# Optimization experiments

Hardware: AMD Instinct MI355X
Metric: run time of the kernel (lower is better)

## Reference

```python
import jax, jax.numpy as jnp
import numpy as np

USER_COUNT = 100000
ITEM_COUNT = 50000
LATENT = 64
N_LAYERS = 3
NEG_SLOPE = 0.2


def _xavier(key, shape):
    fan_in, fan_out = shape[-2], shape[-1]
    lim = jnp.sqrt(6.0 / (fan_in + fan_out))
    return jax.random.uniform(key, shape, jnp.float32, -lim, lim)


def setup_inputs() -> dict:
    key = jax.random.key(0)
    ks = jax.random.split(key, 20)
    E = 2400000
    edge_index = jax.random.randint(ks[0], (2, E), 0, USER_COUNT + ITEM_COUNT, dtype=jnp.int64)
    user = jax.random.randint(ks[1], (4096,), 0, USER_COUNT, dtype=jnp.int64)
    item = jax.random.randint(ks[2], (4096,), 0, ITEM_COUNT, dtype=jnp.int64)
    inp = {"user": user, "item": item, "edge_index": edge_index}
    # online encoder params
    inp["user_emb_o"] = _xavier(ks[3], (USER_COUNT, LATENT))
    inp["item_emb_o"] = _xavier(ks[4], (ITEM_COUNT, LATENT))
    inp["W_o"] = _xavier(ks[5], (N_LAYERS, LATENT, LATENT))
    inp["att_src_o"] = _xavier(ks[6], (N_LAYERS, 1, LATENT))[:, 0, :]
    inp["att_dst_o"] = _xavier(ks[7], (N_LAYERS, 1, LATENT))[:, 0, :]
    inp["bias_o"] = jnp.zeros((N_LAYERS, LATENT), jnp.float32)
    # target encoder params (momentum copy; frozen in torch)
    inp["user_emb_t"] = _xavier(ks[8], (USER_COUNT, LATENT))
    inp["item_emb_t"] = _xavier(ks[9], (ITEM_COUNT, LATENT))
    inp["W_t"] = _xavier(ks[10], (N_LAYERS, LATENT, LATENT))
    inp["att_src_t"] = _xavier(ks[11], (N_LAYERS, 1, LATENT))[:, 0, :]
    inp["att_dst_t"] = _xavier(ks[12], (N_LAYERS, 1, LATENT))[:, 0, :]
    inp["bias_t"] = jnp.zeros((N_LAYERS, LATENT), jnp.float32)
    # predictor Linear(latent, latent)
    inp["pred_W"] = _xavier(ks[13], (LATENT, LATENT))
    inp["pred_b"] = jnp.zeros((LATENT,), jnp.float32)
    return inp


def _gat_conv(x, src, dst, n_nodes, W, a_src, a_dst, b):
    # PyG GATConv, heads=1, concat=True, add_self_loops handled by caller.
    h = x @ W                                   # [N, F]
    e = jax.nn.leaky_relu(jnp.take(h @ a_src, src) + jnp.take(h @ a_dst, dst), NEG_SLOPE)  # [E]
    m = jax.ops.segment_max(e, dst, num_segments=n_nodes)
    m = jnp.where(jnp.isfinite(m), m, 0.0)
    ex = jnp.exp(e - jnp.take(m, dst))
    den = jax.ops.segment_sum(ex, dst, num_segments=n_nodes)
    alpha = ex / jnp.take(den, dst)             # softmax over incoming edges per dst
    msg = alpha[:, None] * jnp.take(h, src, axis=0)  # [E, F]
    return jax.ops.segment_sum(msg, dst, num_segments=n_nodes) + b


def _encode(user_emb, item_emb, W, a_src, a_dst, bias, src, dst):
    x = jnp.concatenate([user_emb, item_emb], axis=0)  # [N, F]
    n_nodes = x.shape[0]
    for l in range(N_LAYERS):
        x = _gat_conv(x, src, dst, n_nodes, W[l], a_src[l], a_dst[l], bias[l])
    return x[:user_emb.shape[0]], x[user_emb.shape[0]:]


def reference(user_emb_o, item_emb_o, W_o, att_src_o, att_dst_o, bias_o,
              user_emb_t, item_emb_t, W_t, att_src_t, att_dst_t, bias_t,
              pred_W, pred_b, user, item, edge_index):
    n_nodes = user_emb_o.shape[0] + item_emb_o.shape[0]
    loops = jnp.arange(n_nodes, dtype=edge_index.dtype)
    src = jnp.concatenate([edge_index[0], loops])  # add self loops (PyG default)
    dst = jnp.concatenate([edge_index[1], loops])
    u_all_o, i_all_o = _encode(user_emb_o, item_emb_o, W_o, att_src_o, att_dst_o, bias_o, src, dst)
    u_all_t, i_all_t = _encode(user_emb_t, item_emb_t, W_t, att_src_t, att_dst_t, bias_t, src, dst)
    u_online = jnp.take(u_all_o, user, axis=0)
    i_online = jnp.take(i_all_o, item, axis=0)
    u_target = jnp.take(u_all_t, user, axis=0)
    i_target = jnp.take(i_all_t, item, axis=0)
    return (u_online @ pred_W.T + pred_b, u_target, i_online @ pred_W.T + pred_b, i_target)
```

## Files before the change

kernel.cpp:

```cpp
#include <hip/hip_runtime.h>
#include <math.h>
#include <stdint.h>

#define LAT 64
#define SLICE 16384
#define BIN_CHUNK 1024

static inline int cdiv(int a, int b) { return (a + b - 1) / b; }

__global__ void k_scan1(const int* __restrict__ cnt, int N, int* __restrict__ out, int* __restrict__ blk_sums) {
    __shared__ int sdata[256];
    int t = threadIdx.x, b = blockIdx.x;
    int base = b * 1024 + t * 4;
    int v[4];
    int s = 0;
#pragma unroll
    for (int u = 0; u < 4; u++) { int i = base + u; v[u] = (i < N) ? cnt[i] : 0; s += v[u]; }
    sdata[t] = s; __syncthreads();
    for (int off = 1; off < 256; off <<= 1) {
        int x = (t >= off) ? sdata[t - off] : 0;
        __syncthreads();
        sdata[t] += x;
        __syncthreads();
    }
    int run = sdata[t] - s;
#pragma unroll
    for (int u = 0; u < 4; u++) { int i = base + u; if (i < N) out[i] = run; run += v[u]; }
    if (t == 255) blk_sums[b] = sdata[255];
}

__global__ void k_scan2(int* __restrict__ blk_sums, int NB) {
    __shared__ int sdata[256];
    int t = threadIdx.x;
    int v = (t < NB) ? blk_sums[t] : 0;
    sdata[t] = v; __syncthreads();
    for (int off = 1; off < 256; off <<= 1) {
        int x = (t >= off) ? sdata[t - off] : 0;
        __syncthreads();
        sdata[t] += x;
        __syncthreads();
    }
    if (t < NB) blk_sums[t] = sdata[t] - v;
}

__global__ void k_scan3(int* __restrict__ row_ptr, const int* __restrict__ blk_offs, int N, int ET) {
    int t = threadIdx.x, b = blockIdx.x;
    int base = b * 1024 + t * 4;
    int off = blk_offs[b];
#pragma unroll
    for (int u = 0; u < 4; u++) { int i = base + u; if (i < N) row_ptr[i] += off; }
    if (b == 0 && t == 0) row_ptr[N] = ET;
}

__global__ __launch_bounds__(256) void k_l0(
        const float* __restrict__ ueo, const float* __restrict__ ieo,
        const float* __restrict__ uet, const float* __restrict__ iet, int NU,
        const float* __restrict__ Wo, const float* __restrict__ Wt,
        const float* __restrict__ atso, const float* __restrict__ atdo,
        const float* __restrict__ atst, const float* __restrict__ atdt,
        float* __restrict__ h2, float* __restrict__ asp, float* __restrict__ adp, int N,
        int gemmGrid, int binGrid,
        const int* __restrict__ src_arr, const int* __restrict__ dst_arr,
        int E, int ET, int rsz, int bcap,
        int2* __restrict__ buckets, int* __restrict__ gcur, int* __restrict__ cnt) {
    __shared__ float sW[64 * 64];
    __shared__ float sX[128 * 65];
    __shared__ float sAs[64], sAd[64];
    int t = threadIdx.x;

    if ((int)blockIdx.x >= gemmGrid) {
        int* lcnt = (int*)sW;
        int* lbase = (int*)sW + 8;
        int bb = blockIdx.x - gemmGrid;
        for (int base = bb * BIN_CHUNK; base < ET; base += binGrid * BIN_CHUNK) {
            if (t < 8) lcnt[t] = 0;
            __syncthreads();
            int s[4], d[4], r[4], lofs[4];
            int nval = 0;
            if (base + BIN_CHUNK <= E) {
                int4 s4 = ((const int4*)(src_arr + base))[t];
                int4 d4 = ((const int4*)(dst_arr + base))[t];
                s[0] = s4.x; s[1] = s4.y; s[2] = s4.z; s[3] = s4.w;
                d[0] = d4.x; d[1] = d4.y; d[2] = d4.z; d[3] = d4.w;
                nval = 4;
            } else {
                for (int k = 0; k < 4; k++) {
                    int e = base + t * 4 + k;
                    if (e < ET) {
                        if (e < E) { s[nval] = src_arr[e]; d[nval] = dst_arr[e]; }
                        else { s[nval] = e - E; d[nval] = e - E; }
                        nval++;
                    }
                }
            }
            for (int k = 0; k < nval; k++) {
                r[k] = d[k] / rsz;
                lofs[k] = atomicAdd(&lcnt[r[k]], 1);
                atomicAdd(&cnt[d[k]], 1);
            }
            __syncthreads();
            if (t < 8) lbase[t] = atomicAdd(&gcur[t], lcnt[t]);
            __syncthreads();
            for (int k = 0; k < nval; k++) {
                buckets[(size_t)r[k] * bcap + lbase[r[k]] + lofs[k]] = make_int2(s[k], d[k]);
            }
            __syncthreads();
        }
        return;
    }

    int enc = blockIdx.x & 1;
    int bb = blockIdx.x >> 1;
    const float* ue = enc ? uet : ueo;
    const float* ie = enc ? iet : ieo;
    const float* W = enc ? Wt : Wo;
    const float* att_s = enc ? atst : atso;
    const float* att_d = enc ? atdt : atdo;
    float* h2e = h2 + enc * 64;
    int row0 = bb * 128;
    {
        const float4* Wv = (const float4*)W;
        float4* sWv = (float4*)sW;
#pragma unroll
        for (int u = 0; u < 4; u++) sWv[t + 256 * u] = Wv[t + 256 * u];
    }
    if (t < 64) { sAs[t] = att_s[t]; sAd[t] = att_d[t]; }
    {
#pragma unroll
        for (int u = 0; u < 8; u++) {
            int idx = t + 256 * u;
            int r = idx >> 4, c4 = idx & 15;
            int grow = row0 + r;
            float4 v = make_float4(0.f, 0.f, 0.f, 0.f);
            if (grow < N) {
                const float* base = (grow < NU) ? ue + (size_t)grow * 64 : ie + (size_t)(grow - NU) * 64;
                v = ((const float4*)base)[c4];
            }
            int cc = c4 * 4;
            sX[r * 65 + cc] = v.x; sX[r * 65 + cc + 1] = v.y; sX[r * 65 + cc + 2] = v.z; sX[r * 65 + cc + 3] = v.w;
        }
    }
    __syncthreads();
    int rl = t >> 2;
    int g = t & 3;
    int c0 = g * 16;
    int rA = rl * 2, rB = rA + 1;
    float accA[16], accB[16];
#pragma unroll
    for (int j = 0; j < 16; j++) { accA[j] = 0.f; accB[j] = 0.f; }
    for (int k = 0; k < 64; k++) {
        float xa = sX[rA * 65 + k];
        float xb = sX[rB * 65 + k];
        const float4* wr = (const float4*)&sW[k * 64 + c0];
        float4 w0 = wr[0], w1 = wr[1], w2 = wr[2], w3 = wr[3];
        accA[0] += xa * w0.x; accA[1] += xa * w0.y; accA[2] += xa * w0.z; accA[3] += xa * w0.w;
        accA[4] += xa * w1.x; accA[5] += xa * w1.y; accA[6] += xa * w1.z; accA[7] += xa * w1.w;
        accA[8] += xa * w2.x; accA[9] += xa * w2.y; accA[10] += xa * w2.z; accA[11] += xa * w2.w;
        accA[12] += xa * w3.x; accA[13] += xa * w3.y; accA[14] += xa * w3.z; accA[15] += xa * w3.w;
        accB[0] += xb * w0.x; accB[1] += xb * w0.y; accB[2] += xb * w0.z; accB[3] += xb * w0.w;
        accB[4] += xb * w1.x; accB[5] += xb * w1.y; accB[6] += xb * w1.z; accB[7] += xb * w1.w;
        accB[8] += xb * w2.x; accB[9] += xb * w2.y; accB[10] += xb * w2.z; accB[11] += xb * w2.w;
        accB[12] += xb * w3.x; accB[13] += xb * w3.y; accB[14] += xb * w3.z; accB[15] += xb * w3.w;
    }
    float sA = 0.f, dA = 0.f, sB = 0.f, dB = 0.f;
#pragma unroll
    for (int j = 0; j < 16; j++) {
        sA += accA[j] * sAs[c0 + j]; dA += accA[j] * sAd[c0 + j];
        sB += accB[j] * sAs[c0 + j]; dB += accB[j] * sAd[c0 + j];
    }
    sA += __shfl_xor(sA, 1); sA += __shfl_xor(sA, 2);
    dA += __shfl_xor(dA, 1); dA += __shfl_xor(dA, 2);
    sB += __shfl_xor(sB, 1); sB += __shfl_xor(sB, 2);
    dB += __shfl_xor(dB, 1); dB += __shfl_xor(dB, 2);
    int rowA = row0 + rA, rowB = row0 + rB;
    if (rowA < N) {
        if (g == 0) { asp[(size_t)rowA * 2 + enc] = sA; adp[(size_t)rowA * 2 + enc] = dA; }
        float4* hv = (float4*)&h2e[(size_t)rowA * 128 + c0];
        hv[0] = make_float4(accA[0], accA[1], accA[2], accA[3]);
        hv[1] = make_float4(accA[4], accA[5], accA[6], accA[7]);
        hv[2] = make_float4(accA[8], accA[9], accA[10], accA[11]);
        hv[3] = make_float4(accA[12], accA[13], accA[14], accA[15]);
    }
    if (rowB < N) {
        if (g == 0) { asp[(size_t)rowB * 2 + enc] = sB; adp[(size_t)rowB * 2 + enc] = dB; }
        float4* hv = (float4*)&h2e[(size_t)rowB * 128 + c0];
        hv[0] = make_float4(accB[0], accB[1], accB[2], accB[3]);
        hv[1] = make_float4(accB[4], accB[5], accB[6], accB[7]);
        hv[2] = make_float4(accB[8], accB[9], accB[10], accB[11]);
        hv[3] = make_float4(accB[12], accB[13], accB[14], accB[15]);
    }
}

__global__ __launch_bounds__(256) void k_binB(const int2* __restrict__ buckets, int bcap,
                                              const int* __restrict__ gcur,
                                              const int* __restrict__ row_ptr, int* __restrict__ cnt,
                                              int* __restrict__ csr_src) {
    int r = blockIdx.x & 7;
    int nb = blockIdx.x >> 3;
    int stride = (gridDim.x >> 3) * 256;
    int total = gcur[r];
    const int* bp = (const int*)(buckets + (size_t)r * bcap);
    for (int i = nb * 256 + threadIdx.x; i < total; i += stride) {
        int s = __builtin_nontemporal_load(bp + 2 * i);
        int d = __builtin_nontemporal_load(bp + 2 * i + 1);
        int pos = atomicAdd(&cnt[d], 1);
        csr_src[row_ptr[d] + pos] = s;
    }
}

__global__ __launch_bounds__(256) void k_gemm2m(const float* __restrict__ xo, const float* __restrict__ xt,
        int NU,
        const float* __restrict__ Wo, const float* __restrict__ Wt,
        const float* __restrict__ atso, const float* __restrict__ atdo,
        const float* __restrict__ atst, const float* __restrict__ atdt,
        float* __restrict__ h2, float* __restrict__ asp, float* __restrict__ adp, int N) {
    __shared__ float sW[64 * 64];
    __shared__ float sX[128 * 65];
    __shared__ float sAs[64], sAd[64];
    int enc = blockIdx.x & 1;
    int bb = blockIdx.x >> 1;
    const float* x = enc ? xt : xo;
    const float* W = enc ? Wt : Wo;
    const float* att_s = enc ? atst : atso;
    const float* att_d = enc ? atdt : atdo;
    float* h2e = h2 + enc * 64;
    int t = threadIdx.x;
    int row0 = bb * 128;
    {
        const float4* Wv = (const float4*)W;
        float4* sWv = (float4*)sW;
#pragma unroll
        for (int u = 0; u < 4; u++) sWv[t + 256 * u] = Wv[t + 256 * u];
    }
    if (t < 64) { sAs[t] = att_s[t]; sAd[t] = att_d[t]; }
    {
#pragma unroll
        for (int u = 0; u < 8; u++) {
            int idx = t + 256 * u;
            int r = idx >> 4, c4 = idx & 15;
            int grow = row0 + r;
            float4 v = make_float4(0.f, 0.f, 0.f, 0.f);
            if (grow < N) v = ((const float4*)(x + (size_t)grow * 64))[c4];
            int cc = c4 * 4;
            sX[r * 65 + cc] = v.x; sX[r * 65 + cc + 1] = v.y; sX[r * 65 + cc + 2] = v.z; sX[r * 65 + cc + 3] = v.w;
        }
    }
    __syncthreads();
    int rl = t >> 2;
    int g = t & 3;
    int c0 = g * 16;
    int rA = rl * 2, rB = rA + 1;
    float accA[16], accB[16];
#pragma unroll
    for (int j = 0; j < 16; j++) { accA[j] = 0.f; accB[j] = 0.f; }
    for (int k = 0; k < 64; k++) {
        float xa = sX[rA * 65 + k];
        float xb = sX[rB * 65 + k];
        const float4* wr = (const float4*)&sW[k * 64 + c0];
        float4 w0 = wr[0], w1 = wr[1], w2 = wr[2], w3 = wr[3];
        accA[0] += xa * w0.x; accA[1] += xa * w0.y; accA[2] += xa * w0.z; accA[3] += xa * w0.w;
        accA[4] += xa * w1.x; accA[5] += xa * w1.y; accA[6] += xa * w1.z; accA[7] += xa * w1.w;
        accA[8] += xa * w2.x; accA[9] += xa * w2.y; accA[10] += xa * w2.z; accA[11] += xa * w2.w;
        accA[12] += xa * w3.x; accA[13] += xa * w3.y; accA[14] += xa * w3.z; accA[15] += xa * w3.w;
        accB[0] += xb * w0.x; accB[1] += xb * w0.y; accB[2] += xb * w0.z; accB[3] += xb * w0.w;
        accB[4] += xb * w1.x; accB[5] += xb * w1.y; accB[6] += xb * w1.z; accB[7] += xb * w1.w;
        accB[8] += xb * w2.x; accB[9] += xb * w2.y; accB[10] += xb * w2.z; accB[11] += xb * w2.w;
        accB[12] += xb * w3.x; accB[13] += xb * w3.y; accB[14] += xb * w3.z; accB[15] += xb * w3.w;
    }
    float sA = 0.f, dA = 0.f, sB = 0.f, dB = 0.f;
#pragma unroll
    for (int j = 0; j < 16; j++) {
        sA += accA[j] * sAs[c0 + j]; dA += accA[j] * sAd[c0 + j];
        sB += accB[j] * sAs[c0 + j]; dB += accB[j] * sAd[c0 + j];
    }
    sA += __shfl_xor(sA, 1); sA += __shfl_xor(sA, 2);
    dA += __shfl_xor(dA, 1); dA += __shfl_xor(dA, 2);
    sB += __shfl_xor(sB, 1); sB += __shfl_xor(sB, 2);
    dB += __shfl_xor(dB, 1); dB += __shfl_xor(dB, 2);
    int rowA = row0 + rA, rowB = row0 + rB;
    if (rowA < N) {
        if (g == 0) { asp[(size_t)rowA * 2 + enc] = sA; adp[(size_t)rowA * 2 + enc] = dA; }
        float4* hv = (float4*)&h2e[(size_t)rowA * 128 + c0];
        hv[0] = make_float4(accA[0], accA[1], accA[2], accA[3]);
        hv[1] = make_float4(accA[4], accA[5], accA[6], accA[7]);
        hv[2] = make_float4(accA[8], accA[9], accA[10], accA[11]);
        hv[3] = make_float4(accA[12], accA[13], accA[14], accA[15]);
    }
    if (rowB < N) {
        if (g == 0) { asp[(size_t)rowB * 2 + enc] = sB; adp[(size_t)rowB * 2 + enc] = dB; }
        float4* hv = (float4*)&h2e[(size_t)rowB * 128 + c0];
        hv[0] = make_float4(accB[0], accB[1], accB[2], accB[3]);
        hv[1] = make_float4(accB[4], accB[5], accB[6], accB[7]);
        hv[2] = make_float4(accB[8], accB[9], accB[10], accB[11]);
        hv[3] = make_float4(accB[12], accB[13], accB[14], accB[15]);
    }
}

__global__ __launch_bounds__(256) void k_agg2(const float* __restrict__ h2,
                                              const int* __restrict__ row_ptr, const int* __restrict__ csr_src,
                                              const float2* __restrict__ asv, const float2* __restrict__ adv,
                                              const float* __restrict__ bias_o, const float* __restrict__ bias_t,
                                              float* __restrict__ xo, float* __restrict__ xt, int N,
                                              const int* __restrict__ selu, const int* __restrict__ seli,
                                              int nSel, int nSelU, int NU,
                                              float* __restrict__ selxo, float* __restrict__ outT_u,
                                              float* __restrict__ outT_i) {
    int wid = threadIdx.x >> 6, lane = threadIdx.x & 63;
    int r = blockIdx.x * 4 + wid;
    int d;
    float *po, *pt;
    if (selu) {
        if (r >= nSel) return;
        if (r < nSelU) { d = selu[r]; pt = outT_u + (size_t)r * 64; }
        else { int rr = r - nSelU; d = seli[rr] + NU; pt = outT_i + (size_t)rr * 64; }
        po = selxo + (size_t)r * 64;
    } else {
        if (r >= N) return;
        d = r;
        po = xo + (size_t)d * 64;
        pt = xt + (size_t)d * 64;
    }
    int s0 = row_ptr[d], s1 = row_ptr[d + 1];
    float2 advv = adv[d];
    int j0 = s0 + lane;
    int sv0 = 0; float eo0 = -1e30f, et0 = -1e30f;
    if (j0 < s1) {
        sv0 = csr_src[j0];
        float2 a2 = asv[sv0];
        float eo = a2.x + advv.x; eo0 = (eo > 0.f) ? eo : 0.2f * eo;
        float et = a2.y + advv.y; et0 = (et > 0.f) ? et : 0.2f * et;
    }
    float mo = eo0, mt = et0;
    for (int j = j0 + 64; j < s1; j += 64) {
        float2 a2 = asv[csr_src[j]];
        float eo = a2.x + advv.x; eo = (eo > 0.f) ? eo : 0.2f * eo; mo = fmaxf(mo, eo);
        float et = a2.y + advv.y; et = (et > 0.f) ? et : 0.2f * et; mt = fmaxf(mt, et);
    }
#pragma unroll
    for (int o = 32; o; o >>= 1) { mo = fmaxf(mo, __shfl_xor(mo, o)); mt = fmaxf(mt, __shfl_xor(mt, o)); }
    float exo0 = (j0 < s1) ? expf(eo0 - mo) : 0.f;
    float ext0 = (j0 < s1) ? expf(et0 - mt) : 0.f;
    float so = exo0, st = ext0;
    for (int j = j0 + 64; j < s1; j += 64) {
        float2 a2 = asv[csr_src[j]];
        float eo = a2.x + advv.x; eo = (eo > 0.f) ? eo : 0.2f * eo; so += expf(eo - mo);
        float et = a2.y + advv.y; et = (et > 0.f) ? et : 0.2f * et; st += expf(et - mt);
    }
#pragma unroll
    for (int o = 32; o; o >>= 1) { so += __shfl_xor(so, o); st += __shfl_xor(st, o); }
    float invo = 1.f / so, invt = 1.f / st;
    exo0 *= invo; ext0 *= invt;
    int sub = lane >> 4, c4 = lane & 15;
    float4 ao = make_float4(0.f, 0.f, 0.f, 0.f);
    float4 at4 = make_float4(0.f, 0.f, 0.f, 0.f);
    for (int cb = s0; cb < s1; cb += 64) {
        int sv; float wo, wt;
        if (cb == s0) { sv = sv0; wo = exo0; wt = ext0; }
        else {
            int jj = cb + lane; sv = 0; wo = 0.f; wt = 0.f;
            if (jj < s1) {
                sv = csr_src[jj];
                float2 a2 = asv[sv];
                float eo = a2.x + advv.x; eo = (eo > 0.f) ? eo : 0.2f * eo; wo = expf(eo - mo) * invo;
                float et = a2.y + advv.y; et = (et > 0.f) ? et : 0.2f * et; wt = expf(et - mt) * invt;
            }
        }
        int c = s1 - cb; if (c > 64) c = 64;
        int q = 0;
        for (; q + 8 <= c; q += 8) {
            int ilA = q + sub, ilB = q + 4 + sub;
            int sA = __shfl(sv, ilA), sB = __shfl(sv, ilB);
            float oA = __shfl(wo, ilA), oB = __shfl(wo, ilB);
            float tA = __shfl(wt, ilA), tB = __shfl(wt, ilB);
            const float* ha = h2 + (size_t)sA * 128 + (c4 << 2);
            const float* hb = h2 + (size_t)sB * 128 + (c4 << 2);
            float4 hoA = *(const float4*)ha;
            float4 htA = *(const float4*)(ha + 64);
            float4 hoB = *(const float4*)hb;
            float4 htB = *(const float4*)(hb + 64);
            ao.x += oA * hoA.x; ao.y += oA * hoA.y; ao.z += oA * hoA.z; ao.w += oA * hoA.w;
            at4.x += tA * htA.x; at4.y += tA * htA.y; at4.z += tA * htA.z; at4.w += tA * htA.w;
            ao.x += oB * hoB.x; ao.y += oB * hoB.y; ao.z += oB * hoB.z; ao.w += oB * hoB.w;
            at4.x += tB * htB.x; at4.y += tB * htB.y; at4.z += tB * htB.z; at4.w += tB * htB.w;
        }
        for (; q < c; q += 4) {
            int il = q + sub;
            int s = __shfl(sv, il);
            float o_ = __shfl(wo, il);
            float t_ = __shfl(wt, il);
            const float* hb = h2 + (size_t)s * 128 + (c4 << 2);
            float4 ho = *(const float4*)hb;
            float4 ht = *(const float4*)(hb + 64);
            ao.x += o_ * ho.x; ao.y += o_ * ho.y; ao.z += o_ * ho.z; ao.w += o_ * ho.w;
            at4.x += t_ * ht.x; at4.y += t_ * ht.y; at4.z += t_ * ht.z; at4.w += t_ * ht.w;
        }
    }
#pragma unroll
    for (int o = 16; o <= 32; o <<= 1) {
        ao.x += __shfl_xor(ao.x, o); ao.y += __shfl_xor(ao.y, o);
        ao.z += __shfl_xor(ao.z, o); ao.w += __shfl_xor(ao.w, o);
        at4.x += __shfl_xor(at4.x, o); at4.y += __shfl_xor(at4.y, o);
        at4.z += __shfl_xor(at4.z, o); at4.w += __shfl_xor(at4.w, o);
    }
    if (lane < 16) {
        float4 bo = ((const float4*)bias_o)[c4];
        ao.x += bo.x; ao.y += bo.y; ao.z += bo.z; ao.w += bo.w;
        ((float4*)po)[c4] = ao;
        float4 bt = ((const float4*)bias_t)[c4];
        at4.x += bt.x; at4.y += bt.y; at4.z += bt.z; at4.w += bt.w;
        ((float4*)pt)[c4] = at4;
    }
}

__global__ __launch_bounds__(256) void k_pred2(const float* __restrict__ x, int nU, int nI,
                                               const float* __restrict__ W, const float* __restrict__ bvec,
                                               float* __restrict__ outU, float* __restrict__ outI) {
    __shared__ float sWt[64 * 65];
    int t = threadIdx.x;
#pragma unroll
    for (int u = 0; u < 16; u++) {
        int i = u * 256 + t;
        int c = i >> 6, k = i & 63;
        sWt[k * 65 + c] = W[i];
    }
    __syncthreads();
    int wid = t >> 6, lane = t & 63;
    int r = blockIdx.x * 4 + wid;
    if (r >= nU + nI) return;
    float xr = x[(size_t)r * 64 + lane];
    float acc = bvec[lane];
    for (int k = 0; k < 64; k++)
        acc += __shfl(xr, k) * sWt[k * 65 + lane];
    float* dst = (r < nU) ? (outU + (size_t)r * 64) : (outI + (size_t)(r - nU) * 64);
    dst[lane] = acc;
}

__global__ void k_count(const int* __restrict__ dst_arr, int E, int N, int* __restrict__ cnt) {
    int e = blockIdx.x * blockDim.x + threadIdx.x;
    int ET = E + N;
    if (e < ET) {
        int d = (e < E) ? dst_arr[e] : (e - E);
        atomicAdd(&cnt[d], 1);
    }
}

__global__ void k_scatter(const int* __restrict__ src_arr, const int* __restrict__ dst_arr, int E, int N,
                          const int* __restrict__ row_ptr, int* __restrict__ cnt, int* __restrict__ csr_src) {
    int ET = E + N;
    int slice = blockIdx.x >> 3;
    int range = blockIdx.x & 7;
    int rsz = (N + 7) >> 3;
    int lo = range * rsz;
    int hi = lo + rsz; if (hi > N) hi = N;
    int base = slice * SLICE;
    int end = base + SLICE; if (end > ET) end = ET;
    for (int e = base + threadIdx.x; e < end; e += 256) {
        int s, d;
        if (e < E) { s = src_arr[e]; d = dst_arr[e]; }
        else { s = e - E; d = e - E; }
        if (d >= lo && d < hi) {
            int pos = atomicAdd(&cnt[d], 1);
            csr_src[row_ptr[d] + pos] = s;
        }
    }
}

__global__ __launch_bounds__(256) void k_gemm(const float* __restrict__ x,
                                              const float* __restrict__ ue, const float* __restrict__ ie, int NU,
                                              const float* __restrict__ W,
                                              const float* __restrict__ att_s, const float* __restrict__ att_d,
                                              float* __restrict__ h, float* __restrict__ as_, float* __restrict__ ad_,
                                              int N) {
    __shared__ float sW[64 * 64];
    __shared__ float sX[128 * 65];
    __shared__ float sAs[64], sAd[64];
    int t = threadIdx.x;
    int row0 = blockIdx.x * 128;
    {
        const float4* Wv = (const float4*)W;
        float4* sWv = (float4*)sW;
#pragma unroll
        for (int u = 0; u < 4; u++) sWv[t + 256 * u] = Wv[t + 256 * u];
    }
    if (t < 64) { sAs[t] = att_s[t]; sAd[t] = att_d[t]; }
    {
#pragma unroll
        for (int u = 0; u < 8; u++) {
            int idx = t + 256 * u;
            int r = idx >> 4, c4 = idx & 15;
            int grow = row0 + r;
            float4 v = make_float4(0.f, 0.f, 0.f, 0.f);
            if (grow < N) {
                const float* base = x ? (x + (size_t)grow * 64)
                                      : (grow < NU ? ue + (size_t)grow * 64 : ie + (size_t)(grow - NU) * 64);
                v = ((const float4*)base)[c4];
            }
            int cc = c4 * 4;
            sX[r * 65 + cc] = v.x; sX[r * 65 + cc + 1] = v.y; sX[r * 65 + cc + 2] = v.z; sX[r * 65 + cc + 3] = v.w;
        }
    }
    __syncthreads();
    int rl = t >> 2;
    int g = t & 3;
    int c0 = g * 16;
    int rA = rl * 2, rB = rA + 1;
    float accA[16], accB[16];
#pragma unroll
    for (int j = 0; j < 16; j++) { accA[j] = 0.f; accB[j] = 0.f; }
    for (int k = 0; k < 64; k++) {
        float xa = sX[rA * 65 + k];
        float xb = sX[rB * 65 + k];
        const float4* wr = (const float4*)&sW[k * 64 + c0];
        float4 w0 = wr[0], w1 = wr[1], w2 = wr[2], w3 = wr[3];
        accA[0] += xa * w0.x; accA[1] += xa * w0.y; accA[2] += xa * w0.z; accA[3] += xa * w0.w;
        accA[4] += xa * w1.x; accA[5] += xa * w1.y; accA[6] += xa * w1.z; accA[7] += xa * w1.w;
        accA[8] += xa * w2.x; accA[9] += xa * w2.y; accA[10] += xa * w2.z; accA[11] += xa * w2.w;
        accA[12] += xa * w3.x; accA[13] += xa * w3.y; accA[14] += xa * w3.z; accA[15] += xa * w3.w;
        accB[0] += xb * w0.x; accB[1] += xb * w0.y; accB[2] += xb * w0.z; accB[3] += xb * w0.w;
        accB[4] += xb * w1.x; accB[5] += xb * w1.y; accB[6] += xb * w1.z; accB[7] += xb * w1.w;
        accB[8] += xb * w2.x; accB[9] += xb * w2.y; accB[10] += xb * w2.z; accB[11] += xb * w2.w;
        accB[12] += xb * w3.x; accB[13] += xb * w3.y; accB[14] += xb * w3.z; accB[15] += xb * w3.w;
    }
    float sA = 0.f, dA = 0.f, sB = 0.f, dB = 0.f;
#pragma unroll
    for (int j = 0; j < 16; j++) {
        sA += accA[j] * sAs[c0 + j]; dA += accA[j] * sAd[c0 + j];
        sB += accB[j] * sAs[c0 + j]; dB += accB[j] * sAd[c0 + j];
    }
    sA += __shfl_xor(sA, 1); sA += __shfl_xor(sA, 2);
    dA += __shfl_xor(dA, 1); dA += __shfl_xor(dA, 2);
    sB += __shfl_xor(sB, 1); sB += __shfl_xor(sB, 2);
    dB += __shfl_xor(dB, 1); dB += __shfl_xor(dB, 2);
    int rowA = row0 + rA, rowB = row0 + rB;
    if (rowA < N) {
        if (g == 0) { as_[rowA] = sA; ad_[rowA] = dA; }
        float4* hv = (float4*)&h[(size_t)rowA * 64 + c0];
        hv[0] = make_float4(accA[0], accA[1], accA[2], accA[3]);
        hv[1] = make_float4(accA[4], accA[5], accA[6], accA[7]);
        hv[2] = make_float4(accA[8], accA[9], accA[10], accA[11]);
        hv[3] = make_float4(accA[12], accA[13], accA[14], accA[15]);
    }
    if (rowB < N) {
        if (g == 0) { as_[rowB] = sB; ad_[rowB] = dB; }
        float4* hv = (float4*)&h[(size_t)rowB * 64 + c0];
        hv[0] = make_float4(accB[0], accB[1], accB[2], accB[3]);
        hv[1] = make_float4(accB[4], accB[5], accB[6], accB[7]);
        hv[2] = make_float4(accB[8], accB[9], accB[10], accB[11]);
        hv[3] = make_float4(accB[12], accB[13], accB[14], accB[15]);
    }
}

__global__ __launch_bounds__(256) void k_agg(const float* __restrict__ h,
                                             const int* __restrict__ row_ptr, const int* __restrict__ csr_src,
                                             const float* __restrict__ as_, const float* __restrict__ ad_,
                                             const float* __restrict__ bias, float* __restrict__ xout, int N) {
    int wid = threadIdx.x >> 6, lane = threadIdx.x & 63;
    int d = blockIdx.x * 4 + wid;
    if (d >= N) return;
    int s0 = row_ptr[d], s1 = row_ptr[d + 1];
    float adv = ad_[d];
    int j0 = s0 + lane;
    int sv0 = 0; float ev0 = -1e30f;
    if (j0 < s1) {
        sv0 = csr_src[j0];
        float e = as_[sv0] + adv;
        ev0 = (e > 0.f) ? e : 0.2f * e;
    }
    float m = ev0;
    for (int j = j0 + 64; j < s1; j += 64) {
        float e = as_[csr_src[j]] + adv;
        e = (e > 0.f) ? e : 0.2f * e;
        m = fmaxf(m, e);
    }
#pragma unroll
    for (int o = 32; o; o >>= 1) m = fmaxf(m, __shfl_xor(m, o));
    float ex0 = (j0 < s1) ? expf(ev0 - m) : 0.f;
    float sum = ex0;
    for (int j = j0 + 64; j < s1; j += 64) {
        float e = as_[csr_src[j]] + adv;
        e = (e > 0.f) ? e : 0.2f * e;
        sum += expf(e - m);
    }
#pragma unroll
    for (int o = 32; o; o >>= 1) sum += __shfl_xor(sum, o);
    float inv = 1.f / sum;
    ex0 *= inv;
    int sub = lane >> 4;
    int c4 = lane & 15;
    float4 acc = make_float4(0.f, 0.f, 0.f, 0.f);
    for (int cbase = s0; cbase < s1; cbase += 64) {
        int sv; float ex;
        if (cbase == s0) { sv = sv0; ex = ex0; }
        else {
            int jj = cbase + lane;
            sv = 0; ex = 0.f;
            if (jj < s1) {
                sv = csr_src[jj];
                float e = as_[sv] + adv;
                e = (e > 0.f) ? e : 0.2f * e;
                ex = expf(e - m) * inv;
            }
        }
        int cnt2 = s1 - cbase; if (cnt2 > 64) cnt2 = 64;
        for (int q = 0; q < cnt2; q += 4) {
            int il = q + sub;
            float w = __shfl(ex, il);
            int s = __shfl(sv, il);
            const float4 hv = *(const float4*)&h[(size_t)s * 64 + (c4 << 2)];
            acc.x += w * hv.x; acc.y += w * hv.y; acc.z += w * hv.z; acc.w += w * hv.w;
        }
    }
#pragma unroll
    for (int o = 16; o <= 32; o <<= 1) {
        acc.x += __shfl_xor(acc.x, o);
        acc.y += __shfl_xor(acc.y, o);
        acc.z += __shfl_xor(acc.z, o);
        acc.w += __shfl_xor(acc.w, o);
    }
    if (lane < 16) {
        float4 bv = ((const float4*)bias)[c4];
        acc.x += bv.x; acc.y += bv.y; acc.z += bv.z; acc.w += bv.w;
        ((float4*)&xout[(size_t)d * 64])[c4] = acc;
    }
}

__global__ __launch_bounds__(256) void k_pred(const float* __restrict__ x, const int* __restrict__ idx,
                                              int nIdx, int rowOff, const float* __restrict__ W,
                                              const float* __restrict__ bvec, float* __restrict__ out) {
    __shared__ float sWt[64 * 65];
    int t = threadIdx.x;
#pragma unroll
    for (int u = 0; u < 16; u++) {
        int i = u * 256 + t;
        int c = i >> 6, k = i & 63;
        sWt[k * 65 + c] = W[i];
    }
    __syncthreads();
    int wid = t >> 6, lane = t & 63;
    int r = blockIdx.x * 4 + wid;
    if (r >= nIdx) return;
    int node = idx ? (idx[r] + rowOff) : (r + rowOff);
    float xr = x[(size_t)node * 64 + lane];
    float acc = bvec[lane];
    for (int k = 0; k < 64; k++)
        acc += __shfl(xr, k) * sWt[k * 65 + lane];
    out[(size_t)r * 64 + lane] = acc;
}

__global__ void k_gather(const float* __restrict__ x, const int* __restrict__ idx, int nIdx, int rowOff,
                         float* __restrict__ out) {
    int t = blockIdx.x * blockDim.x + threadIdx.x;
    if (t < nIdx * 64) {
        int r = t >> 6, c = t & 63;
        int node = idx[r] + rowOff;
        out[t] = x[(size_t)node * 64 + c];
    }
}

extern "C" void kernel_launch(void* const* d_in, const int* in_sizes, int n_in,
                              void* d_out, int out_size, void* d_ws, size_t ws_size,
                              hipStream_t stream) {
    const int* user = (const int*)d_in[0];
    const int* item = (const int*)d_in[1];
    const int* edge = (const int*)d_in[2];
    const float* user_emb_o = (const float*)d_in[3];
    const float* item_emb_o = (const float*)d_in[4];
    const float* W_o = (const float*)d_in[5];
    const float* att_src_o = (const float*)d_in[6];
    const float* att_dst_o = (const float*)d_in[7];
    const float* bias_o = (const float*)d_in[8];
    const float* user_emb_t = (const float*)d_in[9];
    const float* item_emb_t = (const float*)d_in[10];
    const float* W_t = (const float*)d_in[11];
    const float* att_src_t = (const float*)d_in[12];
    const float* att_dst_t = (const float*)d_in[13];
    const float* bias_t = (const float*)d_in[14];
    const float* pred_W = (const float*)d_in[15];
    const float* pred_b = (const float*)d_in[16];
    float* out = (float*)d_out;

    int E = in_sizes[2] / 2;
    int NU = in_sizes[3] / LAT;
    int NI = in_sizes[4] / LAT;
    int N = NU + NI;
    int ET = E + N;
    int nU = in_sizes[0];
    int nI = in_sizes[1];
    int nSel = nU + nI;
    int rsz = (N + 7) >> 3;

    const int* src_arr = edge;
    const int* dst_arr = edge + E;

    auto al = [](size_t v) { return (v + 255) & ~(size_t)255; };

    char* p = (char*)d_ws;
    float* x_o   = (float*)p;  p += al((size_t)N * LAT * 4);
    float* x_t   = (float*)p;  p += al((size_t)N * LAT * 4);
    float* h2    = (float*)p;  p += al((size_t)N * 2 * LAT * 4);
    float* asv   = (float*)p;  p += al((size_t)N * 8);
    float* adv   = (float*)p;  p += al((size_t)N * 8);
    int* row_ptr = (int*)p;    p += al((size_t)(N + 1) * 4);
    int* cnt     = (int*)p;    size_t cntsz = al((size_t)N * 4); p += cntsz;
    int* gcur    = (int*)p;    p += al(64);
    int* csr_src = (int*)p;    p += al((size_t)ET * 4);
    int* blk     = (int*)p;    p += al(4096);
    float* xsel  = (float*)p;  p += al((size_t)nSel * LAT * 4);
    size_t need_primary = (size_t)(p - (char*)d_ws);

    int bcap = ET / 8 + 16384;
    int2* buckets = (int2*)x_o;

    bool primary = ws_size >= need_primary;

    if (primary) {
        int gemmGrid = cdiv(N, 128) * 2;
        int binGrid = 1024;
        hipMemsetAsync(cnt, 0, cntsz + 64, stream);
        k_l0<<<gemmGrid + binGrid, 256, 0, stream>>>(
                user_emb_o, item_emb_o, user_emb_t, item_emb_t, NU,
                W_o, W_t, att_src_o, att_dst_o, att_src_t, att_dst_t,
                h2, asv, adv, N,
                gemmGrid, binGrid,
                src_arr, dst_arr, E, ET, rsz, bcap,
                buckets, gcur, cnt);
        int NB = cdiv(N, 1024);
        k_scan1<<<NB, 256, 0, stream>>>(cnt, N, row_ptr, blk);
        k_scan2<<<1, 256, 0, stream>>>(blk, NB);
        k_scan3<<<NB, 256, 0, stream>>>(row_ptr, blk, N, ET);
        hipMemsetAsync(cnt, 0, (size_t)N * 4, stream);
        k_binB<<<1024, 256, 0, stream>>>(buckets, bcap, gcur, row_ptr, cnt, csr_src);

        for (int l = 0; l < 3; l++) {
            if (l > 0) {
                k_gemm2m<<<cdiv(N, 128) * 2, 256, 0, stream>>>(x_o, x_t, NU,
                        W_o + l * 4096, W_t + l * 4096,
                        att_src_o + l * 64, att_dst_o + l * 64,
                        att_src_t + l * 64, att_dst_t + l * 64,
                        h2, asv, adv, N);
            }
            if (l < 2) {
                k_agg2<<<cdiv(N, 4), 256, 0, stream>>>(h2, row_ptr, csr_src,
                        (const float2*)asv, (const float2*)adv,
                        bias_o + l * 64, bias_t + l * 64,
                        x_o, x_t, N,
                        nullptr, nullptr, 0, 0, NU, nullptr, nullptr, nullptr);
            } else {
                k_agg2<<<cdiv(nSel, 4), 256, 0, stream>>>(h2, row_ptr, csr_src,
                        (const float2*)asv, (const float2*)adv,
                        bias_o + l * 64, bias_t + l * 64,
                        nullptr, nullptr, N,
                        user, item, nSel, nU, NU,
                        xsel, out + (size_t)nU * LAT, out + (size_t)3 * nU * LAT);
            }
        }
        k_pred2<<<cdiv(nSel, 4), 256, 0, stream>>>(xsel, nU, nI, pred_W, pred_b,
                                                   out, out + (size_t)2 * nU * LAT);
        return;
    }

    p = (char*)d_ws;
    float* x_cur = (float*)p;  p += al((size_t)N * LAT * 4);
    float* h     = (float*)p;  p += al((size_t)N * LAT * 4);
    float* as_   = (float*)p;  p += al((size_t)N * 4);
    float* ad_   = (float*)p;  p += al((size_t)N * 4);
    row_ptr = (int*)p;         p += al((size_t)(N + 1) * 4);
    cnt     = (int*)p;         p += al((size_t)N * 4);
    csr_src = (int*)p;         p += al((size_t)ET * 4);
    blk     = (int*)p;         p += al(4096);

    hipMemsetAsync(cnt, 0, (size_t)N * 4, stream);
    k_count<<<cdiv(ET, 256), 256, 0, stream>>>(dst_arr, E, N, cnt);
    int NB = cdiv(N, 1024);
    k_scan1<<<NB, 256, 0, stream>>>(cnt, N, row_ptr, blk);
    k_scan2<<<1, 256, 0, stream>>>(blk, NB);
    k_scan3<<<NB, 256, 0, stream>>>(row_ptr, blk, N, ET);
    hipMemsetAsync(cnt, 0, (size_t)N * 4, stream);
    k_scatter<<<cdiv(ET, SLICE) * 8, 256, 0, stream>>>(src_arr, dst_arr, E, N, row_ptr, cnt, csr_src);

    auto run_encoder = [&](const float* ue, const float* ie, const float* Wl,
                           const float* asl, const float* adl, const float* bl) {
        for (int l = 0; l < 3; l++) {
            const float* xin = (l == 0) ? nullptr : x_cur;
            k_gemm<<<cdiv(N, 128), 256, 0, stream>>>(xin, ue, ie, NU, Wl + l * 64 * 64, asl + l * 64,
                                                     adl + l * 64, h, as_, ad_, N);
            k_agg<<<cdiv(N, 4), 256, 0, stream>>>(h, row_ptr, csr_src, as_, ad_, bl + l * 64, x_cur, N);
        }
    };

    run_encoder(user_emb_o, item_emb_o, W_o, att_src_o, att_dst_o, bias_o);
    k_pred<<<cdiv(nU, 4), 256, 0, stream>>>(x_cur, user, nU, 0, pred_W, pred_b, out);
    k_pred<<<cdiv(nI, 4), 256, 0, stream>>>(x_cur, item, nI, NU, pred_W, pred_b, out + (size_t)2 * nU * LAT);

    run_encoder(user_emb_t, item_emb_t, W_t, att_src_t, att_dst_t, bias_t);
    k_gather<<<cdiv(nU * LAT, 256), 256, 0, stream>>>(x_cur, user, nU, 0, out + (size_t)nU * LAT);
    k_gather<<<cdiv(nI * LAT, 256), 256, 0, stream>>>(x_cur, item, nI, NU, out + (size_t)3 * nU * LAT);
}
```

Measured before the change: 837.2 us.

## Fuse GAT aggregation with next layer's linear transform and attention scores

```diff
diff --git a/kernel.cpp b/kernel.cpp
--- a/kernel.cpp
+++ b/kernel.cpp
@@ -208,91 +208,117 @@
     }
 }
 
-__global__ __launch_bounds__(256) void k_gemm2m(const float* __restrict__ xo, const float* __restrict__ xt,
-        int NU,
-        const float* __restrict__ Wo, const float* __restrict__ Wt,
-        const float* __restrict__ atso, const float* __restrict__ atdo,
-        const float* __restrict__ atst, const float* __restrict__ atdt,
-        float* __restrict__ h2, float* __restrict__ asp, float* __restrict__ adp, int N) {
-    __shared__ float sW[64 * 64];
-    __shared__ float sX[128 * 65];
-    __shared__ float sAs[64], sAd[64];
+__global__ __launch_bounds__(256) void k_fagg(const float* __restrict__ h2_in,
+        const int* __restrict__ row_ptr, const int* __restrict__ csr_src,
+        const float* __restrict__ asv_in, const float* __restrict__ adv_in,
+        const float* __restrict__ bias_o, const float* __restrict__ bias_t,
+        const float* __restrict__ Wn_o, const float* __restrict__ Wn_t,
+        const float* __restrict__ atsn_o, const float* __restrict__ atdn_o,
+        const float* __restrict__ atsn_t, const float* __restrict__ atdn_t,
+        float* __restrict__ h2_out, float* __restrict__ asv_out, float* __restrict__ adv_out,
+        int N) {
+    __shared__ float sW[64 * 65];
     int enc = blockIdx.x & 1;
     int bb = blockIdx.x >> 1;
-    const float* x = enc ? xt : xo;
-    const float* W = enc ? Wt : Wo;
-    const float* att_s = enc ? atst : atso;
-    const float* att_d = enc ? atdt : atdo;
-    float* h2e = h2 + enc * 64;
     int t = threadIdx.x;
-    int row0 = bb * 128;
-    {
-        const float4* Wv = (const float4*)W;
-        float4* sWv = (float4*)sW;
-#pragma unroll
-        for (int u = 0; u < 4; u++) sWv[t + 256 * u] = Wv[t + 256 * u];
-    }
-    if (t < 64) { sAs[t] = att_s[t]; sAd[t] = att_d[t]; }
-    {
-#pragma unroll
-        for (int u = 0; u < 8; u++) {
-            int idx = t + 256 * u;
-            int r = idx >> 4, c4 = idx & 15;
-            int grow = row0 + r;
-            float4 v = make_float4(0.f, 0.f, 0.f, 0.f);
-            if (grow < N) v = ((const float4*)(x + (size_t)grow * 64))[c4];
-            int cc = c4 * 4;
-            sX[r * 65 + cc] = v.x; sX[r * 65 + cc + 1] = v.y; sX[r * 65 + cc + 2] = v.z; sX[r * 65 + cc + 3] = v.w;
-        }
-    }
+    const float* Wn = enc ? Wn_t : Wn_o;
+#pragma unroll
+    for (int u = 0; u < 16; u++) {
+        int i = u * 256 + t;
+        int k = i >> 6, c = i & 63;
+        sW[c * 65 + k] = Wn[i];
+    }
+    int wid = t >> 6, lane = t & 63;
+    int d = bb * 4 + wid;
+    float attS = (enc ? atsn_t : atsn_o)[lane];
+    float attD = (enc ? atdn_t : atdn_o)[lane];
+    int c4 = lane & 15, sub = lane >> 4;
+    float4 bias4 = ((const float4*)(enc ? bias_t : bias_o))[c4];
     __syncthreads();
-    int rl = t >> 2;
-    int g = t & 3;
-    int c0 = g * 16;
-    int rA = rl * 2, rB = rA + 1;
-    float accA[16], accB[16];
-#pragma unroll
-    for (int j = 0; j < 16; j++) { accA[j] = 0.f; accB[j] = 0.f; }
-    for (int k = 0; k < 64; k++) {
-        float xa = sX[rA * 65 + k];
-        float xb = sX[rB * 65 + k];
-        const float4* wr = (const float4*)&sW[k * 64 + c0];
-        float4 w0 = wr[0], w1 = wr[1], w2 = wr[2], w3 = wr[3];
-        accA[0] += xa * w0.x; accA[1] += xa * w0.y; accA[2] += xa * w0.z; accA[3] += xa * w0.w;
-        accA[4] += xa * w1.x; accA[5] += xa * w1.y; accA[6] += xa * w1.z; accA[7] += xa * w1.w;
-        accA[8] += xa * w2.x; accA[9] += xa * w2.y; accA[10] += xa * w2.z; accA[11] += xa * w2.w;
-        accA[12] += xa * w3.x; accA[13] += xa * w3.y; accA[14] += xa * w3.z; accA[15] += xa * w3.w;
-        accB[0] += xb * w0.x; accB[1] += xb * w0.y; accB[2] += xb * w0.z; accB[3] += xb * w0.w;
-        accB[4] += xb * w1.x; accB[5] += xb * w1.y; accB[6] += xb * w1.z; accB[7] += xb * w1.w;
-        accB[8] += xb * w2.x; accB[9] += xb * w2.y; accB[10] += xb * w2.z; accB[11] += xb * w2.w;
-        accB[12] += xb * w3.x; accB[13] += xb * w3.y; accB[14] += xb * w3.z; accB[15] += xb * w3.w;
-    }
-    float sA = 0.f, dA = 0.f, sB = 0.f, dB = 0.f;
-#pragma unroll
-    for (int j = 0; j < 16; j++) {
-        sA += accA[j] * sAs[c0 + j]; dA += accA[j] * sAd[c0 + j];
-        sB += accB[j] * sAs[c0 + j]; dB += accB[j] * sAd[c0 + j];
-    }
-    sA += __shfl_xor(sA, 1); sA += __shfl_xor(sA, 2);
-    dA += __shfl_xor(dA, 1); dA += __shfl_xor(dA, 2);
-    sB += __shfl_xor(sB, 1); sB += __shfl_xor(sB, 2);
-    dB += __shfl_xor(dB, 1); dB += __shfl_xor(dB, 2);
-    int rowA = row0 + rA, rowB = row0 + rB;
-    if (rowA < N) {
-        if (g == 0) { asp[(size_t)rowA * 2 + enc] = sA; adp[(size_t)rowA * 2 + enc] = dA; }
-        float4* hv = (float4*)&h2e[(size_t)rowA * 128 + c0];
-        hv[0] = make_float4(accA[0], accA[1], accA[2], accA[3]);
-        hv[1] = make_float4(accA[4], accA[5], accA[6], accA[7]);
-        hv[2] = make_float4(accA[8], accA[9], accA[10], accA[11]);
-        hv[3] = make_float4(accA[12], accA[13], accA[14], accA[15]);
-    }
-    if (rowB < N) {
-        if (g == 0) { asp[(size_t)rowB * 2 + enc] = sB; adp[(size_t)rowB * 2 + enc] = dB; }
-        float4* hv = (float4*)&h2e[(size_t)rowB * 128 + c0];
-        hv[0] = make_float4(accB[0], accB[1], accB[2], accB[3]);
-        hv[1] = make_float4(accB[4], accB[5], accB[6], accB[7]);
-        hv[2] = make_float4(accB[8], accB[9], accB[10], accB[11]);
-        hv[3] = make_float4(accB[12], accB[13], accB[14], accB[15]);
+    if (d >= N) return;
+
+    int s0 = row_ptr[d], s1 = row_ptr[d + 1];
+    float advv = adv_in[(size_t)d * 2 + enc];
+    int j0 = s0 + lane;
+    int sv0 = 0; float e0 = -1e30f;
+    if (j0 < s1) {
+        sv0 = csr_src[j0];
+        float e = asv_in[(size_t)sv0 * 2 + enc] + advv;
+        e0 = (e > 0.f) ? e : 0.2f * e;
+    }
+    float m = e0;
+    for (int j = j0 + 64; j < s1; j += 64) {
+        float e = asv_in[(size_t)csr_src[j] * 2 + enc] + advv;
+        e = (e > 0.f) ? e : 0.2f * e;
+        m = fmaxf(m, e);
+    }
+#pragma unroll
+    for (int o = 32; o; o >>= 1) m = fmaxf(m, __shfl_xor(m, o));
+    float ex0 = (j0 < s1) ? expf(e0 - m) : 0.f;
+    float sum = ex0;
+    for (int j = j0 + 64; j < s1; j += 64) {
+        float e = asv_in[(size_t)csr_src[j] * 2 + enc] + advv;
+        e = (e > 0.f) ? e : 0.2f * e;
+        sum += expf(e - m);
+    }
+#pragma unroll
+    for (int o = 32; o; o >>= 1) sum += __shfl_xor(sum, o);
+    float inv = 1.f / sum;
+    ex0 *= inv;
+    float4 acc = make_float4(0.f, 0.f, 0.f, 0.f);
+    for (int cb = s0; cb < s1; cb += 64) {
+        int sv; float ex;
+        if (cb == s0) { sv = sv0; ex = ex0; }
+        else {
+            int jj = cb + lane; sv = 0; ex = 0.f;
+            if (jj < s1) {
+                sv = csr_src[jj];
+                float e = asv_in[(size_t)sv * 2 + enc] + advv;
+                e = (e > 0.f) ? e : 0.2f * e;
+                ex = expf(e - m) * inv;
+            }
+        }
+        int c = s1 - cb; if (c > 64) c = 64;
+        int q = 0;
+        for (; q + 8 <= c; q += 8) {
+            int ilA = q + sub, ilB = q + 4 + sub;
+            int sA = __shfl(sv, ilA), sB = __shfl(sv, ilB);
+            float wA = __shfl(ex, ilA), wB = __shfl(ex, ilB);
+            float4 hA = *(const float4*)&h2_in[(size_t)sA * 128 + enc * 64 + (c4 << 2)];
+            float4 hB = *(const float4*)&h2_in[(size_t)sB * 128 + enc * 64 + (c4 << 2)];
+            acc.x += wA * hA.x; acc.y += wA * hA.y; acc.z += wA * hA.z; acc.w += wA * hA.w;
+            acc.x += wB * hB.x; acc.y += wB * hB.y; acc.z += wB * hB.z; acc.w += wB * hB.w;
+        }
+        for (; q < c; q += 4) {
+            int il = q + sub;
+            int s = __shfl(sv, il);
+            float w = __shfl(ex, il);
+            float4 hv = *(const float4*)&h2_in[(size_t)s * 128 + enc * 64 + (c4 << 2)];
+            acc.x += w * hv.x; acc.y += w * hv.y; acc.z += w * hv.z; acc.w += w * hv.w;
+        }
+    }
+#pragma unroll
+    for (int o = 16; o <= 32; o <<= 1) {
+        acc.x += __shfl_xor(acc.x, o); acc.y += __shfl_xor(acc.y, o);
+        acc.z += __shfl_xor(acc.z, o); acc.w += __shfl_xor(acc.w, o);
+    }
+    float4 xr;
+    xr.x = acc.x + bias4.x; xr.y = acc.y + bias4.y;
+    xr.z = acc.z + bias4.z; xr.w = acc.w + bias4.w;
+    float hacc = 0.f;
+#pragma unroll
+    for (int k4 = 0; k4 < 16; k4++) {
+        const float4 wv = *(const float4*)&sW[lane * 65 + k4 * 4];
+        hacc += __shfl(xr.x, k4) * wv.x + __shfl(xr.y, k4) * wv.y +
+                __shfl(xr.z, k4) * wv.z + __shfl(xr.w, k4) * wv.w;
+    }
+    float so = hacc * attS, sd = hacc * attD;
+#pragma unroll
+    for (int o = 32; o; o >>= 1) { so += __shfl_xor(so, o); sd += __shfl_xor(sd, o); }
+    h2_out[(size_t)d * 128 + enc * 64 + lane] = hacc;
+    if (lane == 0) {
+        asv_out[(size_t)d * 2 + enc] = so;
+        adv_out[(size_t)d * 2 + enc] = sd;
     }
 }
 
@@ -695,11 +721,12 @@
     auto al = [](size_t v) { return (v + 255) & ~(size_t)255; };
 
     char* p = (char*)d_ws;
-    float* x_o   = (float*)p;  p += al((size_t)N * LAT * 4);
-    float* x_t   = (float*)p;  p += al((size_t)N * LAT * 4);
-    float* h2    = (float*)p;  p += al((size_t)N * 2 * LAT * 4);
-    float* asv   = (float*)p;  p += al((size_t)N * 8);
-    float* adv   = (float*)p;  p += al((size_t)N * 8);
+    float* h2a   = (float*)p;  p += al((size_t)N * 2 * LAT * 4);
+    float* h2b   = (float*)p;  p += al((size_t)N * 2 * LAT * 4);
+    float* asa   = (float*)p;  p += al((size_t)N * 8);
+    float* ada   = (float*)p;  p += al((size_t)N * 8);
+    float* asb   = (float*)p;  p += al((size_t)N * 8);
+    float* adb   = (float*)p;  p += al((size_t)N * 8);
     int* row_ptr = (int*)p;    p += al((size_t)(N + 1) * 4);
     int* cnt     = (int*)p;    size_t cntsz = al((size_t)N * 4); p += cntsz;
     int* gcur    = (int*)p;    p += al(64);
@@ -709,7 +736,7 @@
     size_t need_primary = (size_t)(p - (char*)d_ws);
 
     int bcap = ET / 8 + 16384;
-    int2* buckets = (int2*)x_o;
+    int2* buckets = (int2*)h2b;
 
     bool primary = ws_size >= need_primary;
 
@@ -720,7 +747,7 @@
         k_l0<<<gemmGrid + binGrid, 256, 0, stream>>>(
                 user_emb_o, item_emb_o, user_emb_t, item_emb_t, NU,
                 W_o, W_t, att_src_o, att_dst_o, att_src_t, att_dst_t,
-                h2, asv, adv, N,
+                h2a, asa, ada, N,
                 gemmGrid, binGrid,
                 src_arr, dst_arr, E, ET, rsz, bcap,
                 buckets, gcur, cnt);
@@ -731,29 +758,22 @@
         hipMemsetAsync(cnt, 0, (size_t)N * 4, stream);
         k_binB<<<1024, 256, 0, stream>>>(buckets, bcap, gcur, row_ptr, cnt, csr_src);
 
-        for (int l = 0; l < 3; l++) {
-            if (l > 0) {
-                k_gemm2m<<<cdiv(N, 128) * 2, 256, 0, stream>>>(x_o, x_t, NU,
-                        W_o + l * 4096, W_t + l * 4096,
-                        att_src_o + l * 64, att_dst_o + l * 64,
-                        att_src_t + l * 64, att_dst_t + l * 64,
-                        h2, asv, adv, N);
-            }
-            if (l < 2) {
-                k_agg2<<<cdiv(N, 4), 256, 0, stream>>>(h2, row_ptr, csr_src,
-                        (const float2*)asv, (const float2*)adv,
-                        bias_o + l * 64, bias_t + l * 64,
-                        x_o, x_t, N,
-                        nullptr, nullptr, 0, 0, NU, nullptr, nullptr, nullptr);
-            } else {
-                k_agg2<<<cdiv(nSel, 4), 256, 0, stream>>>(h2, row_ptr, csr_src,
-                        (const float2*)asv, (const float2*)adv,
-                        bias_o + l * 64, bias_t + l * 64,
-                        nullptr, nullptr, N,
-                        user, item, nSel, nU, NU,
-                        xsel, out + (size_t)nU * LAT, out + (size_t)3 * nU * LAT);
-            }
-        }
+        k_fagg<<<cdiv(N, 4) * 2, 256, 0, stream>>>(h2a, row_ptr, csr_src, asa, ada,
+                bias_o, bias_t,
+                W_o + 4096, W_t + 4096,
+                att_src_o + 64, att_dst_o + 64, att_src_t + 64, att_dst_t + 64,
+                h2b, asb, adb, N);
+        k_fagg<<<cdiv(N, 4) * 2, 256, 0, stream>>>(h2b, row_ptr, csr_src, asb, adb,
+                bias_o + 64, bias_t + 64,
+                W_o + 2 * 4096, W_t + 2 * 4096,
+                att_src_o + 128, att_dst_o + 128, att_src_t + 128, att_dst_t + 128,
+                h2a, asa, ada, N);
+        k_agg2<<<cdiv(nSel, 4), 256, 0, stream>>>(h2a, row_ptr, csr_src,
+                (const float2*)asa, (const float2*)ada,
+                bias_o + 128, bias_t + 128,
+                nullptr, nullptr, N,
+                user, item, nSel, nU, NU,
+                xsel, out + (size_t)nU * LAT, out + (size_t)3 * nU * LAT);
         k_pred2<<<cdiv(nSel, 4), 256, 0, stream>>>(xsel, nU, nI, pred_W, pred_b,
                                                    out, out + (size_t)2 * nU * LAT);
         return;
```

Result: slower. 1.152 ms (+37.6%).
